# Kernel optimization log

Measured on AMD Instinct MI355X. Metric: run time of the kernel, lower is better.

Reference implementation:

```python
import jax, jax.numpy as jnp
import numpy as np

N, F, H, T = 100000, 128, 128, 10
E = 1600000
NUM_GRAPHS = 512
BN_EPS = 1e-5


def setup_inputs() -> dict:
    key = jax.random.key(0)
    ks = jax.random.split(key, 16)
    x = jax.random.normal(ks[0], (N, F), dtype=jnp.float32)
    edge_index = jax.random.randint(ks[1], (2, E), 0, N, dtype=jnp.int64)
    batch = jnp.sort(jax.random.randint(ks[2], (N,), 0, NUM_GRAPHS, dtype=jnp.int64))
    s = lambda fin: 1.0 / np.sqrt(fin)
    return {
        "x": x, "edge_index": edge_index, "batch": batch,
        # GINConv 1 MLP: Linear(F,H) -> BN(H) -> ReLU -> Linear(H,H)
        "W1a": jax.random.uniform(ks[3], (F, H), jnp.float32, -s(F), s(F)),
        "b1a": jax.random.uniform(ks[4], (H,), jnp.float32, -s(F), s(F)),
        "g1": jnp.ones((H,), jnp.float32),
        "bt1": jnp.zeros((H,), jnp.float32),
        "W1b": jax.random.uniform(ks[5], (H, H), jnp.float32, -s(H), s(H)),
        "b1b": jax.random.uniform(ks[6], (H,), jnp.float32, -s(H), s(H)),
        # GINConv 2 MLP
        "W2a": jax.random.uniform(ks[7], (H, H), jnp.float32, -s(H), s(H)),
        "b2a": jax.random.uniform(ks[8], (H,), jnp.float32, -s(H), s(H)),
        "g2": jnp.ones((H,), jnp.float32),
        "bt2": jnp.zeros((H,), jnp.float32),
        "W2b": jax.random.uniform(ks[9], (H, H), jnp.float32, -s(H), s(H)),
        "b2b": jax.random.uniform(ks[10], (H,), jnp.float32, -s(H), s(H)),
        # final Linear(H, T)
        "Wl": jax.random.uniform(ks[11], (H, T), jnp.float32, -s(H), s(H)),
        "bl": jax.random.uniform(ks[12], (T,), jnp.float32, -s(H), s(H)),
    }


def _batchnorm(h, gamma, beta):
    # training-mode BN over the node dimension (biased variance), eps=1e-5
    mean = jnp.mean(h, axis=0)
    var = jnp.mean(jnp.square(h - mean), axis=0)
    return (h - mean) * jax.lax.rsqrt(var + BN_EPS) * gamma + beta


def _gin_conv(x, edge_index, Wa, ba, gamma, beta, Wb, bb):
    src, dst = edge_index[0], edge_index[1]
    # sum-aggregate neighbor messages: scatter-add x[src] into dst rows
    agg = jax.ops.segment_sum(x[src], dst, num_segments=x.shape[0])
    h = (x + agg) @ Wa + ba          # eps=0 in GINConv default
    h = jax.nn.relu(_batchnorm(h, gamma, beta))
    return h @ Wb + bb


def reference(x, edge_index, batch, W1a, b1a, g1, bt1, W1b, b1b,
              W2a, b2a, g2, bt2, W2b, b2b, Wl, bl):
    h = jax.nn.relu(_gin_conv(x, edge_index, W1a, b1a, g1, bt1, W1b, b1b))
    h = jax.nn.relu(_gin_conv(h, edge_index, W2a, b2a, g2, bt2, W2b, b2b))
    pooled = jax.ops.segment_sum(h, batch, num_segments=NUM_GRAPHS)  # [G, H]
    return pooled @ Wl + bl  # [G, T]
```

## Files before the change

kernel.cpp:

```cpp
#include <hip/hip_runtime.h>
#include <cstdint>
#include <cstddef>

#define NFEAT 128
#define TGRAPH 10
#define NGRAPHS 512
#define BN_EPS 1e-5f
#define BIN_CHUNK 2048
#define GSPAN 8
#define TSTR 24

typedef __attribute__((ext_vector_type(8))) short bf16x8;
typedef __attribute__((ext_vector_type(4))) float f32x4;
typedef __attribute__((ext_vector_type(2))) float f32x2;

__device__ __forceinline__ float bf2f(short s) {
    union { unsigned u; float f; } c;
    c.u = ((unsigned)(unsigned short)s) << 16;
    return c.f;
}
__device__ __forceinline__ short f2bf(float f) {
    union { float f; unsigned u; } c;
    c.f = f;
    unsigned u = c.u;
    return (short)((u + 0x7fffu + ((u >> 16) & 1u)) >> 16);
}
__device__ __forceinline__ void accp(f32x2& a, unsigned v) {
    union { unsigned u; float f; } lo, hi;
    lo.u = v << 16;
    hi.u = v & 0xffff0000u;
    f32x2 t;
    t[0] = lo.f;
    t[1] = hi.f;
    a += t;
}


__global__ void k_bucket_scan(const int* __restrict__ bhist, int* __restrict__ bbase,
                              int* __restrict__ cur256, int E) {
    __shared__ int s[256];
    int t = threadIdx.x;
    int v = bhist[t];
    s[t] = v;
    __syncthreads();
    for (int off = 1; off < 256; off <<= 1) {
        int x = 0;
        if (t >= off) x = s[t - off];
        __syncthreads();
        if (t >= off) s[t] += x;
        __syncthreads();
    }
    int excl = s[t] - v;
    bbase[t] = excl;
    cur256[t] = excl;
    if (t == 255) bbase[256] = E;
}

__global__ __launch_bounds__(256) void k_bin_scatter(const int* __restrict__ src,
                                                     const int* __restrict__ dst,
                                                     int* __restrict__ cur256,
                                                     int2* __restrict__ binned, int E) {
    __shared__ int hist[256];
    __shared__ int base[256];
    int t = threadIdx.x;
    int e0 = blockIdx.x * BIN_CHUNK;
    int e1 = min(e0 + BIN_CHUNK, E);
    hist[t] = 0;
    __syncthreads();
    for (int e = e0 + t; e < e1; e += 256) {
        int b = dst[e] >> 9;
        atomicAdd(&hist[b], 1);
    }
    __syncthreads();
    int c = hist[t];
    if (c > 0) base[t] = atomicAdd(&cur256[t], c);
    __syncthreads();
    hist[t] = 0;
    __syncthreads();
    for (int e = e0 + t; e < e1; e += 256) {
        int d = dst[e];
        int b = d >> 9;
        int loc = atomicAdd(&hist[b], 1);
        binned[base[b] + loc] = make_int2(src[e], d);
    }
}

__global__ __launch_bounds__(512) void k_bucket_csr(const int2* __restrict__ binned,
                                                    const int* __restrict__ bbase,
                                                    int* __restrict__ rowptr,
                                                    int* __restrict__ adj,
                                                    int N, int E, int nb) {
    __shared__ int deg[512];
    __shared__ int cur[512];
    int b = blockIdx.x;
    int t = threadIdx.x;
    int e0 = bbase[b], e1 = bbase[b + 1];
    deg[t] = 0;
    __syncthreads();
    for (int e = e0 + t; e < e1; e += 512)
        atomicAdd(&deg[binned[e].y & 511], 1);
    __syncthreads();
    int v = deg[t];
    for (int off = 1; off < 512; off <<= 1) {
        int x = 0;
        if (t >= off) x = deg[t - off];
        __syncthreads();
        if (t >= off) deg[t] += x;
        __syncthreads();
    }
    int excl = deg[t] - v;
    cur[t] = excl;
    int node = b * 512 + t;
    if (node < N) rowptr[node] = e0 + excl;
    if (b == nb - 1 && t == 0) rowptr[N] = E;
    __syncthreads();
    for (int e = e0 + t; e < e1; e += 512) {
        int2 p = binned[e];
        int loc = atomicAdd(&cur[p.y & 511], 1);
        adj[e0 + loc] = p.x;
    }
}

__global__ __launch_bounds__(256) void k_prep_hist(const int* __restrict__ dst,
                                                   int* __restrict__ bhist, int E, int hb,
                                                   const float* __restrict__ x,
                                                   short* __restrict__ xbf,
                                                   const float* __restrict__ W0,
                                                   const float* __restrict__ W1,
                                                   const float* __restrict__ W2,
                                                   const float* __restrict__ W3,
                                                   short* __restrict__ Wf, int n4) {
    int t = threadIdx.x;
    if (blockIdx.x < hb) {
        __shared__ int h[256];
        h[t] = 0;
        __syncthreads();
        for (int e = blockIdx.x * 256 + t; e < E; e += hb * 256)
            atomicAdd(&h[dst[e] >> 9], 1);
        __syncthreads();
        if (h[t]) atomicAdd(&bhist[t], h[t]);
        return;
    }
    int i = (blockIdx.x - hb) * 256 + t;
    if (i < n4) {
        float4 v = ((const float4*)x)[i];
        ushort4 o;
        o.x = (unsigned short)f2bf(v.x);
        o.y = (unsigned short)f2bf(v.y);
        o.z = (unsigned short)f2bf(v.z);
        o.w = (unsigned short)f2bf(v.w);
        ((ushort4*)xbf)[i] = o;
    } else {
        int idx = i - n4;
        if (idx < 4 * 16384) {
            int w = idx >> 14, r = idx & 16383;
            int j = r & 7, lane = (r >> 3) & 63, ct = (r >> 9) & 7, kc = r >> 12;
            int k = kc * 32 + (lane >> 4) * 8 + j;
            int n = ct * 16 + (lane & 15);
            const float* W = (w == 0) ? W0 : (w == 1) ? W1 : (w == 2) ? W2 : W3;
            Wf[idx] = f2bf(W[k * NFEAT + n]);
        }
    }
}

__global__ __launch_bounds__(256) void k_aggregate_v4(const short* __restrict__ X,
                                                      const int* __restrict__ rowptr,
                                                      const int* __restrict__ adj,
                                                      short* __restrict__ XA, int N) {
    int tid = threadIdx.x;
    int lane = tid & 63;
    int g = lane >> 4;
    int p = lane & 15;
    int wid = (blockIdx.x * blockDim.x + tid) >> 6;
    if (wid >= N) return;
    const uint4* Xv = (const uint4*)X;
    f32x2 ac[4];
#pragma unroll
    for (int j = 0; j < 4; j++) ac[j] = (f32x2){0.f, 0.f};
    int r0 = rowptr[wid], r1 = rowptr[wid + 1];
    for (int e = r0; e < r1; e += 16) {
        int ea = e + g, eb = e + 4 + g, ec = e + 8 + g, ed = e + 12 + g;
        uint4 v0 = {0u, 0u, 0u, 0u}, v1 = {0u, 0u, 0u, 0u};
        uint4 v2 = {0u, 0u, 0u, 0u}, v3 = {0u, 0u, 0u, 0u};
        if (ea < r1) v0 = Xv[(size_t)adj[ea] * 16 + p];
        if (eb < r1) v1 = Xv[(size_t)adj[eb] * 16 + p];
        if (ec < r1) v2 = Xv[(size_t)adj[ec] * 16 + p];
        if (ed < r1) v3 = Xv[(size_t)adj[ed] * 16 + p];
        accp(ac[0], v0.x); accp(ac[1], v0.y); accp(ac[2], v0.z); accp(ac[3], v0.w);
        accp(ac[0], v1.x); accp(ac[1], v1.y); accp(ac[2], v1.z); accp(ac[3], v1.w);
        accp(ac[0], v2.x); accp(ac[1], v2.y); accp(ac[2], v2.z); accp(ac[3], v2.w);
        accp(ac[0], v3.x); accp(ac[1], v3.y); accp(ac[2], v3.z); accp(ac[3], v3.w);
    }
#pragma unroll
    for (int j = 0; j < 4; j++) {
        ac[j][0] += __shfl_xor(ac[j][0], 16);
        ac[j][1] += __shfl_xor(ac[j][1], 16);
        ac[j][0] += __shfl_xor(ac[j][0], 32);
        ac[j][1] += __shfl_xor(ac[j][1], 32);
    }
    if (g == 0) {
        uint4 sv = Xv[(size_t)wid * 16 + p];
        accp(ac[0], sv.x); accp(ac[1], sv.y); accp(ac[2], sv.z); accp(ac[3], sv.w);
        uint4 o;
        o.x = (unsigned)(unsigned short)f2bf(ac[0][0]) | ((unsigned)(unsigned short)f2bf(ac[0][1]) << 16);
        o.y = (unsigned)(unsigned short)f2bf(ac[1][0]) | ((unsigned)(unsigned short)f2bf(ac[1][1]) << 16);
        o.z = (unsigned)(unsigned short)f2bf(ac[2][0]) | ((unsigned)(unsigned short)f2bf(ac[2][1]) << 16);
        o.w = (unsigned)(unsigned short)f2bf(ac[3][0]) | ((unsigned)(unsigned short)f2bf(ac[3][1]) << 16);
        size_t dst = ((size_t)(wid >> 4) * 4 + (p >> 2)) * 512 +
                     (size_t)(((p & 3) * 16 + (wid & 15)) * 8);
        *(uint4*)(XA + dst) = o;
    }
}

template <bool BN_RELU_IN, bool RELU_OUT, bool STATS, bool FRAG_OUT, bool POOL>
__global__ __launch_bounds__(256) void k_gemm_mfma(const short* __restrict__ A,
                                                   const short* __restrict__ Wf,
                                                   const float* __restrict__ bias,
                                                   float* __restrict__ stats,
                                                   const float* __restrict__ gamma,
                                                   const float* __restrict__ beta,
                                                   const int* __restrict__ batch,
                                                   float* __restrict__ pooled,
                                                   short* __restrict__ C, int N) {
    __shared__ float s_aux[256];
    __shared__ short c_tile[4][32 * TSTR];
    __shared__ float s_pool[GSPAN][NFEAT];
    int tid = threadIdx.x;
    int wave = tid >> 6, lane = tid & 63;
    int quad = lane >> 4, l16 = lane & 15;
    int row_base = blockIdx.x * 128 + wave * 32;

    int gbase = 0;
    if constexpr (POOL) {
        int first = blockIdx.x * 128;
        gbase = (first < N) ? batch[first] : 0;
        for (int i = tid; i < GSPAN * NFEAT; i += 256) s_pool[i >> 7][i & 127] = 0.f;
    }
    if constexpr (STATS) s_aux[tid] = 0.f;
    if constexpr (BN_RELU_IN) {
        if (tid < NFEAT) {
            float mean = stats[tid] / (float)N;
            float var = stats[NFEAT + tid] / (float)N - mean * mean;
            float inv = rsqrtf(var + BN_EPS);
            float sc = gamma[tid] * inv;
            s_aux[tid] = sc;
            s_aux[NFEAT + tid] = beta[tid] - mean * sc;
        }
    }
    if constexpr (STATS || BN_RELU_IN || POOL) __syncthreads();

    f32x4 acc[2][8];
#pragma unroll
    for (int i = 0; i < 2; i++)
#pragma unroll
        for (int j = 0; j < 8; j++) acc[i][j] = (f32x4){0.f, 0.f, 0.f, 0.f};

    const short* af = A + ((size_t)(blockIdx.x * 8 + wave * 2) * 4) * 512;

#pragma unroll
    for (int kc = 0; kc < 4; ++kc) {
        bf16x8 a0 = *(const bf16x8*)(af + (size_t)kc * 512 + lane * 8);
        bf16x8 a1 = *(const bf16x8*)(af + (size_t)(4 + kc) * 512 + lane * 8);
        if constexpr (BN_RELU_IN) {
            int koff = kc * 32 + quad * 8;
#pragma unroll
            for (int j = 0; j < 8; j++) {
                float sc = s_aux[koff + j];
                float sh = s_aux[NFEAT + koff + j];
                a0[j] = f2bf(fmaxf(bf2f(a0[j]) * sc + sh, 0.f));
                a1[j] = f2bf(fmaxf(bf2f(a1[j]) * sc + sh, 0.f));
            }
        }
        const short* wp = Wf + ((size_t)(kc * 8) * 64 + lane) * 8;
#pragma unroll
        for (int ct = 0; ct < 8; ++ct) {
            bf16x8 b = *(const bf16x8*)(wp + (size_t)ct * 64 * 8);
            acc[0][ct] = __builtin_amdgcn_mfma_f32_16x16x32_bf16(a0, b, acc[0][ct], 0, 0, 0);
            acc[1][ct] = __builtin_amdgcn_mfma_f32_16x16x32_bf16(a1, b, acc[1][ct], 0, 0, 0);
        }
    }

    int dg[8];
    if constexpr (POOL) {
#pragma unroll
        for (int rt = 0; rt < 2; ++rt)
#pragma unroll
            for (int reg = 0; reg < 4; ++reg) {
                int row = row_base + rt * 16 + quad * 4 + reg;
                dg[rt * 4 + reg] = (row < N) ? (batch[row] - gbase) : -1;
            }
    }

    short* tile = &c_tile[wave][0];
    int row2 = lane >> 1, half = lane & 1;
#pragma unroll
    for (int ct = 0; ct < 8; ++ct) {
        int col = ct * 16 + l16;
        float bv = bias[col];
        float ls = 0.f, ls2 = 0.f;
        int cg = -1;
        float ps = 0.f;
#pragma unroll
        for (int rt = 0; rt < 2; ++rt) {
#pragma unroll
            for (int reg = 0; reg < 4; ++reg) {
                int lrow = rt * 16 + quad * 4 + reg;
                float v = acc[rt][ct][reg] + bv;
                if constexpr (RELU_OUT) v = fmaxf(v, 0.f);
                if constexpr (STATS) {
                    if (row_base + lrow < N) { ls += v; ls2 += v * v; }
                }
                if constexpr (POOL) {
                    int d = dg[rt * 4 + reg];
                    if (d != cg) {
                        if (cg >= 0) atomicAdd(&s_pool[cg & (GSPAN - 1)][col], ps);
                        cg = d; ps = 0.f;
                    }
                    if (d >= 0) ps += v;
                } else {
                    tile[lrow * TSTR + l16] = f2bf(v);
                }
            }
        }
        if constexpr (POOL) {
            if (cg >= 0) atomicAdd(&s_pool[cg & (GSPAN - 1)][col], ps);
        }
        if constexpr (STATS) {
            ls += __shfl_xor(ls, 16);
            ls += __shfl_xor(ls, 32);
            ls2 += __shfl_xor(ls2, 16);
            ls2 += __shfl_xor(ls2, 32);
            if (quad == 0) {
                atomicAdd(&s_aux[col], ls);
                atomicAdd(&s_aux[NFEAT + col], ls2);
            }
        }
        if constexpr (!POOL) {
            uint4 val = *(const uint4*)(tile + row2 * TSTR + half * 8);
            int grow = row_base + row2;
            if (grow < N) {
                int col0 = ct * 16 + half * 8;
                if constexpr (FRAG_OUT) {
                    size_t addr = ((size_t)(grow >> 4) * 4 + (col0 >> 5)) * 512 +
                                  (size_t)((((col0 >> 3) & 3) * 16 + (grow & 15)) * 8);
                    *(uint4*)(C + addr) = val;
                } else {
                    *(uint4*)(C + (size_t)grow * NFEAT + col0) = val;
                }
            }
        }
    }

    if constexpr (STATS) {
        __syncthreads();
        if (tid < NFEAT) {
            atomicAdd(&stats[tid], s_aux[tid]);
            atomicAdd(&stats[NFEAT + tid], s_aux[NFEAT + tid]);
        }
    }
    if constexpr (POOL) {
        __syncthreads();
        for (int i = tid; i < GSPAN * NFEAT; i += 256) {
            float v = s_pool[i >> 7][i & 127];
            if (v != 0.f) {
                int gg = gbase + (i >> 7);
                if (gg < NGRAPHS) atomicAdd(&pooled[gg * NFEAT + (i & 127)], v);
            }
        }
    }
}

__global__ void k_final(const float* __restrict__ pooled, const float* __restrict__ Wl,
                        const float* __restrict__ bl, float* __restrict__ out) {
    int idx = blockIdx.x * blockDim.x + threadIdx.x;
    if (idx >= NGRAPHS * TGRAPH) return;
    int g = idx / TGRAPH, t = idx % TGRAPH;
    const float* p = pooled + (size_t)g * NFEAT;
    float acc = bl[t];
#pragma unroll 16
    for (int k = 0; k < NFEAT; ++k) acc += p[k] * Wl[k * TGRAPH + t];
    out[idx] = acc;
}

extern "C" void kernel_launch(void* const* d_in, const int* in_sizes, int n_in,
                              void* d_out, int out_size, void* d_ws, size_t ws_size,
                              hipStream_t stream) {
    const float* x = (const float*)d_in[0];
    const int* ei = (const int*)d_in[1];
    const int* batch = (const int*)d_in[2];
    const float* W1a = (const float*)d_in[3];
    const float* b1a = (const float*)d_in[4];
    const float* g1 = (const float*)d_in[5];
    const float* bt1 = (const float*)d_in[6];
    const float* W1b = (const float*)d_in[7];
    const float* b1b = (const float*)d_in[8];
    const float* W2a = (const float*)d_in[9];
    const float* b2a = (const float*)d_in[10];
    const float* g2 = (const float*)d_in[11];
    const float* bt2 = (const float*)d_in[12];
    const float* W2b = (const float*)d_in[13];
    const float* b2b = (const float*)d_in[14];
    const float* Wl = (const float*)d_in[15];
    const float* bl = (const float*)d_in[16];
    float* out = (float*)d_out;

    int N = in_sizes[2];
    int E = in_sizes[1] / 2;
    int nb = (N + 511) >> 9;
    const int* src = ei;
    const int* dst = ei + E;

    int gemmBlocks = (N + 127) / 128;
    int padRows = gemmBlocks * 128;

    char* ws = (char*)d_ws;
    size_t off = 0;
    auto alloc = [&](size_t bytes) -> void* {
        void* p = ws + off;
        off = (off + bytes + 255) & ~(size_t)255;
        return p;
    };
    short* xbf = (short*)alloc((size_t)N * NFEAT * 2);
    short* ag = (short*)alloc((size_t)padRows * NFEAT * 2);
    short* ybf = (short*)alloc((size_t)padRows * NFEAT * 2);
    short* hbf = (short*)alloc((size_t)N * NFEAT * 2);
    short* Wf = (short*)alloc((size_t)4 * 16384 * 2);
    int* adj = (int*)alloc((size_t)E * 4);
    int2* binned = (int2*)alloc((size_t)E * 8);
    int* rowptr = (int*)alloc((size_t)(N + 1) * 4);
    int* bbase = (int*)alloc(257 * 4);
    int* cur256 = (int*)alloc(256 * 4);
    int* bhist = (int*)alloc(256 * 4);
    float* stats1 = (float*)alloc(256 * 4);
    float* stats2 = (float*)alloc(256 * 4);
    float* pooled = (float*)alloc((size_t)NGRAPHS * NFEAT * 4);
    size_t zbytes = (char*)(pooled + (size_t)NGRAPHS * NFEAT) - (char*)bhist;

    hipMemsetAsync(bhist, 0, zbytes, stream);

    int n4 = N * NFEAT / 4;
    int prepTot = n4 + 4 * 16384;
    int hb = 784;
    k_prep_hist<<<hb + (prepTot + 255) / 256, 256, 0, stream>>>(
        dst, bhist, E, hb, x, xbf, W1a, W1b, W2a, W2b, Wf, n4);
    k_bucket_scan<<<1, 256, 0, stream>>>(bhist, bbase, cur256, E);
    k_bin_scatter<<<(E + BIN_CHUNK - 1) / BIN_CHUNK, 256, 0, stream>>>(src, dst, cur256, binned, E);
    k_bucket_csr<<<nb, 512, 0, stream>>>(binned, bbase, rowptr, adj, N, E, nb);

    int aggBlocks = (N + 3) / 4;

    k_aggregate_v4<<<aggBlocks, 256, 0, stream>>>(xbf, rowptr, adj, ag, N);
    k_gemm_mfma<false, false, true, true, false><<<gemmBlocks, 256, 0, stream>>>(
        ag, Wf + 0 * 16384, b1a, stats1, nullptr, nullptr, nullptr, nullptr, ybf, N);
    k_gemm_mfma<true, true, false, false, false><<<gemmBlocks, 256, 0, stream>>>(
        ybf, Wf + 1 * 16384, b1b, stats1, g1, bt1, nullptr, nullptr, hbf, N);

    k_aggregate_v4<<<aggBlocks, 256, 0, stream>>>(hbf, rowptr, adj, ag, N);
    k_gemm_mfma<false, false, true, true, false><<<gemmBlocks, 256, 0, stream>>>(
        ag, Wf + 2 * 16384, b2a, stats2, nullptr, nullptr, nullptr, nullptr, ybf, N);
    k_gemm_mfma<true, true, false, false, true><<<gemmBlocks, 256, 0, stream>>>(
        ybf, Wf + 3 * 16384, b2b, stats2, g2, bt2, batch, pooled, nullptr, N);

    k_final<<<(NGRAPHS * TGRAPH + 255) / 256, 256, 0, stream>>>(pooled, Wl, bl, out);
}
```

Measured before the change: 440.9 us.

## Fuse neighbor aggregation into the first MLP GEMM of each GIN layer

Replaces the separate aggregation kernel and first GEMM with one kernel. Each lane gathers and sums neighbor rows straight into MFMA A-fragments in registers, then runs the bf16 MFMA and writes out bias, BN statistics and fragment-layout output. This removes the intermediate aggregated buffer round-trip through memory and one launch per layer. The trade-off is less memory-level parallelism in the gather: each lane walks a row's edges serially, and the grid is much smaller than the per-node-wave aggregation.

```diff
diff --git a/kernel.cpp b/kernel.cpp
--- a/kernel.cpp
+++ b/kernel.cpp
@@ -163,52 +163,137 @@
     }
 }
 
-__global__ __launch_bounds__(256) void k_aggregate_v4(const short* __restrict__ X,
-                                                      const int* __restrict__ rowptr,
-                                                      const int* __restrict__ adj,
-                                                      short* __restrict__ XA, int N) {
+__global__ __launch_bounds__(256) void k_agg_gemm(const short* __restrict__ X,
+                                                  const int* __restrict__ rowptr,
+                                                  const int* __restrict__ adj,
+                                                  const short* __restrict__ Wf,
+                                                  const float* __restrict__ bias,
+                                                  float* __restrict__ stats,
+                                                  short* __restrict__ C, int N) {
+    __shared__ float s_aux[256];
+    __shared__ short c_tile[4][32 * TSTR];
     int tid = threadIdx.x;
-    int lane = tid & 63;
-    int g = lane >> 4;
-    int p = lane & 15;
-    int wid = (blockIdx.x * blockDim.x + tid) >> 6;
-    if (wid >= N) return;
+    int wave = tid >> 6, lane = tid & 63;
+    int quad = lane >> 4, l16 = lane & 15;
+    int row_base = blockIdx.x * 128 + wave * 32;
+
+    s_aux[tid] = 0.f;
+    __syncthreads();
+
     const uint4* Xv = (const uint4*)X;
-    f32x2 ac[4];
-#pragma unroll
-    for (int j = 0; j < 4; j++) ac[j] = (f32x2){0.f, 0.f};
-    int r0 = rowptr[wid], r1 = rowptr[wid + 1];
-    for (int e = r0; e < r1; e += 16) {
-        int ea = e + g, eb = e + 4 + g, ec = e + 8 + g, ed = e + 12 + g;
-        uint4 v0 = {0u, 0u, 0u, 0u}, v1 = {0u, 0u, 0u, 0u};
-        uint4 v2 = {0u, 0u, 0u, 0u}, v3 = {0u, 0u, 0u, 0u};
-        if (ea < r1) v0 = Xv[(size_t)adj[ea] * 16 + p];
-        if (eb < r1) v1 = Xv[(size_t)adj[eb] * 16 + p];
-        if (ec < r1) v2 = Xv[(size_t)adj[ec] * 16 + p];
-        if (ed < r1) v3 = Xv[(size_t)adj[ed] * 16 + p];
-        accp(ac[0], v0.x); accp(ac[1], v0.y); accp(ac[2], v0.z); accp(ac[3], v0.w);
-        accp(ac[0], v1.x); accp(ac[1], v1.y); accp(ac[2], v1.z); accp(ac[3], v1.w);
-        accp(ac[0], v2.x); accp(ac[1], v2.y); accp(ac[2], v2.z); accp(ac[3], v2.w);
-        accp(ac[0], v3.x); accp(ac[1], v3.y); accp(ac[2], v3.z); accp(ac[3], v3.w);
-    }
-#pragma unroll
-    for (int j = 0; j < 4; j++) {
-        ac[j][0] += __shfl_xor(ac[j][0], 16);
-        ac[j][1] += __shfl_xor(ac[j][1], 16);
-        ac[j][0] += __shfl_xor(ac[j][0], 32);
-        ac[j][1] += __shfl_xor(ac[j][1], 32);
-    }
-    if (g == 0) {
-        uint4 sv = Xv[(size_t)wid * 16 + p];
-        accp(ac[0], sv.x); accp(ac[1], sv.y); accp(ac[2], sv.z); accp(ac[3], sv.w);
-        uint4 o;
-        o.x = (unsigned)(unsigned short)f2bf(ac[0][0]) | ((unsigned)(unsigned short)f2bf(ac[0][1]) << 16);
-        o.y = (unsigned)(unsigned short)f2bf(ac[1][0]) | ((unsigned)(unsigned short)f2bf(ac[1][1]) << 16);
-        o.z = (unsigned)(unsigned short)f2bf(ac[2][0]) | ((unsigned)(unsigned short)f2bf(ac[2][1]) << 16);
-        o.w = (unsigned)(unsigned short)f2bf(ac[3][0]) | ((unsigned)(unsigned short)f2bf(ac[3][1]) << 16);
-        size_t dst = ((size_t)(wid >> 4) * 4 + (p >> 2)) * 512 +
-                     (size_t)(((p & 3) * 16 + (wid & 15)) * 8);
-        *(uint4*)(XA + dst) = o;
+
+    bf16x8 afrag[2][4];
+#pragma unroll
+    for (int rt = 0; rt < 2; ++rt) {
+        f32x2 acc[4][4];
+#pragma unroll
+        for (int kc = 0; kc < 4; ++kc)
+#pragma unroll
+            for (int m = 0; m < 4; ++m) acc[kc][m] = (f32x2){0.f, 0.f};
+        int r = row_base + rt * 16 + l16;
+        if (r < N) {
+            size_t rb = (size_t)r * 16 + quad;
+#pragma unroll
+            for (int kc = 0; kc < 4; ++kc) {
+                uint4 v = Xv[rb + kc * 4];
+                accp(acc[kc][0], v.x); accp(acc[kc][1], v.y);
+                accp(acc[kc][2], v.z); accp(acc[kc][3], v.w);
+            }
+            int e = rowptr[r], e1 = rowptr[r + 1];
+            for (; e + 2 <= e1; e += 2) {
+                size_t n0 = (size_t)adj[e] * 16 + quad;
+                size_t n1 = (size_t)adj[e + 1] * 16 + quad;
+                uint4 u0[4], u1[4];
+#pragma unroll
+                for (int kc = 0; kc < 4; ++kc) u0[kc] = Xv[n0 + kc * 4];
+#pragma unroll
+                for (int kc = 0; kc < 4; ++kc) u1[kc] = Xv[n1 + kc * 4];
+#pragma unroll
+                for (int kc = 0; kc < 4; ++kc) {
+                    accp(acc[kc][0], u0[kc].x); accp(acc[kc][1], u0[kc].y);
+                    accp(acc[kc][2], u0[kc].z); accp(acc[kc][3], u0[kc].w);
+                    accp(acc[kc][0], u1[kc].x); accp(acc[kc][1], u1[kc].y);
+                    accp(acc[kc][2], u1[kc].z); accp(acc[kc][3], u1[kc].w);
+                }
+            }
+            if (e < e1) {
+                size_t n0 = (size_t)adj[e] * 16 + quad;
+#pragma unroll
+                for (int kc = 0; kc < 4; ++kc) {
+                    uint4 v = Xv[n0 + kc * 4];
+                    accp(acc[kc][0], v.x); accp(acc[kc][1], v.y);
+                    accp(acc[kc][2], v.z); accp(acc[kc][3], v.w);
+                }
+            }
+        }
+#pragma unroll
+        for (int kc = 0; kc < 4; ++kc) {
+            bf16x8 f;
+#pragma unroll
+            for (int m = 0; m < 4; ++m) {
+                f[2 * m] = f2bf(acc[kc][m][0]);
+                f[2 * m + 1] = f2bf(acc[kc][m][1]);
+            }
+            afrag[rt][kc] = f;
+        }
+    }
+
+    f32x4 acc[2][8];
+#pragma unroll
+    for (int i = 0; i < 2; i++)
+#pragma unroll
+        for (int j = 0; j < 8; j++) acc[i][j] = (f32x4){0.f, 0.f, 0.f, 0.f};
+
+#pragma unroll
+    for (int kc = 0; kc < 4; ++kc) {
+        const short* wp = Wf + ((size_t)(kc * 8) * 64 + lane) * 8;
+#pragma unroll
+        for (int ct = 0; ct < 8; ++ct) {
+            bf16x8 b = *(const bf16x8*)(wp + (size_t)ct * 64 * 8);
+            acc[0][ct] = __builtin_amdgcn_mfma_f32_16x16x32_bf16(afrag[0][kc], b, acc[0][ct], 0, 0, 0);
+            acc[1][ct] = __builtin_amdgcn_mfma_f32_16x16x32_bf16(afrag[1][kc], b, acc[1][ct], 0, 0, 0);
+        }
+    }
+
+    short* tile = &c_tile[wave][0];
+    int row2 = lane >> 1, half = lane & 1;
+#pragma unroll
+    for (int ct = 0; ct < 8; ++ct) {
+        int col = ct * 16 + l16;
+        float bv = bias[col];
+        float ls = 0.f, ls2 = 0.f;
+#pragma unroll
+        for (int rt = 0; rt < 2; ++rt) {
+#pragma unroll
+            for (int reg = 0; reg < 4; ++reg) {
+                int lrow = rt * 16 + quad * 4 + reg;
+                float v = acc[rt][ct][reg] + bv;
+                if (row_base + lrow < N) { ls += v; ls2 += v * v; }
+                tile[lrow * TSTR + l16] = f2bf(v);
+            }
+        }
+        ls += __shfl_xor(ls, 16);
+        ls += __shfl_xor(ls, 32);
+        ls2 += __shfl_xor(ls2, 16);
+        ls2 += __shfl_xor(ls2, 32);
+        if (quad == 0) {
+            atomicAdd(&s_aux[col], ls);
+            atomicAdd(&s_aux[NFEAT + col], ls2);
+        }
+        uint4 val = *(const uint4*)(tile + row2 * TSTR + half * 8);
+        int grow = row_base + row2;
+        if (grow < N) {
+            int col0 = ct * 16 + half * 8;
+            size_t addr = ((size_t)(grow >> 4) * 4 + (col0 >> 5)) * 512 +
+                          (size_t)((((col0 >> 3) & 3) * 16 + (grow & 15)) * 8);
+            *(uint4*)(C + addr) = val;
+        }
+    }
+
+    __syncthreads();
+    if (tid < NFEAT) {
+        atomicAdd(&stats[tid], s_aux[tid]);
+        atomicAdd(&stats[NFEAT + tid], s_aux[NFEAT + tid]);
     }
 }
 
@@ -421,7 +506,6 @@
         return p;
     };
     short* xbf = (short*)alloc((size_t)N * NFEAT * 2);
-    short* ag = (short*)alloc((size_t)padRows * NFEAT * 2);
     short* ybf = (short*)alloc((size_t)padRows * NFEAT * 2);
     short* hbf = (short*)alloc((size_t)N * NFEAT * 2);
     short* Wf = (short*)alloc((size_t)4 * 16384 * 2);
@@ -447,17 +531,13 @@
     k_bin_scatter<<<(E + BIN_CHUNK - 1) / BIN_CHUNK, 256, 0, stream>>>(src, dst, cur256, binned, E);
     k_bucket_csr<<<nb, 512, 0, stream>>>(binned, bbase, rowptr, adj, N, E, nb);
 
-    int aggBlocks = (N + 3) / 4;
-
-    k_aggregate_v4<<<aggBlocks, 256, 0, stream>>>(xbf, rowptr, adj, ag, N);
-    k_gemm_mfma<false, false, true, true, false><<<gemmBlocks, 256, 0, stream>>>(
-        ag, Wf + 0 * 16384, b1a, stats1, nullptr, nullptr, nullptr, nullptr, ybf, N);
+    k_agg_gemm<<<gemmBlocks, 256, 0, stream>>>(xbf, rowptr, adj, Wf + 0 * 16384, b1a,
+                                               stats1, ybf, N);
     k_gemm_mfma<true, true, false, false, false><<<gemmBlocks, 256, 0, stream>>>(
         ybf, Wf + 1 * 16384, b1b, stats1, g1, bt1, nullptr, nullptr, hbf, N);
 
-    k_aggregate_v4<<<aggBlocks, 256, 0, stream>>>(hbf, rowptr, adj, ag, N);
-    k_gemm_mfma<false, false, true, true, false><<<gemmBlocks, 256, 0, stream>>>(
-        ag, Wf + 2 * 16384, b2a, stats2, nullptr, nullptr, nullptr, nullptr, ybf, N);
+    k_agg_gemm<<<gemmBlocks, 256, 0, stream>>>(hbf, rowptr, adj, Wf + 2 * 16384, b2a,
+                                               stats2, ybf, N);
     k_gemm_mfma<true, true, false, false, true><<<gemmBlocks, 256, 0, stream>>>(
         ybf, Wf + 3 * 16384, b2b, stats2, g2, bt2, batch, pooled, nullptr, N);
 
```

New measurement: 452.4 us. 1.03x slower.

## Fuse neighbor aggregation with first MLP GEMM and BN stats

Applied to the files above, without the earlier changes.

Replaces the separate aggregation kernel and first GEMM with one kernel. Each 1024-thread block aggregates 16 rows into shared memory, then 8 waves run MFMA for the 16x128 output tile, add bias, accumulate batch-norm statistics and write fragment-layout output. This removes the round trip of the aggregated intermediate through global memory and one launch per layer. In exchange it adds a block-wide sync per 16 rows and many more stats atomics, since blocks now cover 16 rows instead of 128.

```diff
diff --git a/kernel.cpp b/kernel.cpp
--- a/kernel.cpp
+++ b/kernel.cpp
@@ -163,33 +163,40 @@
     }
 }
 
-__global__ __launch_bounds__(256) void k_aggregate_v4(const short* __restrict__ X,
-                                                      const int* __restrict__ rowptr,
-                                                      const int* __restrict__ adj,
-                                                      short* __restrict__ XA, int N) {
+__global__ __launch_bounds__(1024, 8) void k_agg_gemm_a(const short* __restrict__ X,
+                                                        const int* __restrict__ rowptr,
+                                                        const int* __restrict__ adj,
+                                                        const short* __restrict__ Wf,
+                                                        const float* __restrict__ bias,
+                                                        float* __restrict__ stats,
+                                                        short* __restrict__ C, int N) {
+    __shared__ __align__(16) short arow[16][136];
+    __shared__ __align__(16) short c_tile[8][16 * TSTR];
+    __shared__ float s_aux[256];
     int tid = threadIdx.x;
-    int lane = tid & 63;
-    int g = lane >> 4;
-    int p = lane & 15;
-    int wid = (blockIdx.x * blockDim.x + tid) >> 6;
-    if (wid >= N) return;
+    int wave = tid >> 6, lane = tid & 63;
+    int g = lane >> 4, p = lane & 15;
+    int wid = blockIdx.x * 16 + wave;
+
     const uint4* Xv = (const uint4*)X;
     f32x2 ac[4];
 #pragma unroll
     for (int j = 0; j < 4; j++) ac[j] = (f32x2){0.f, 0.f};
-    int r0 = rowptr[wid], r1 = rowptr[wid + 1];
-    for (int e = r0; e < r1; e += 16) {
-        int ea = e + g, eb = e + 4 + g, ec = e + 8 + g, ed = e + 12 + g;
-        uint4 v0 = {0u, 0u, 0u, 0u}, v1 = {0u, 0u, 0u, 0u};
-        uint4 v2 = {0u, 0u, 0u, 0u}, v3 = {0u, 0u, 0u, 0u};
-        if (ea < r1) v0 = Xv[(size_t)adj[ea] * 16 + p];
-        if (eb < r1) v1 = Xv[(size_t)adj[eb] * 16 + p];
-        if (ec < r1) v2 = Xv[(size_t)adj[ec] * 16 + p];
-        if (ed < r1) v3 = Xv[(size_t)adj[ed] * 16 + p];
-        accp(ac[0], v0.x); accp(ac[1], v0.y); accp(ac[2], v0.z); accp(ac[3], v0.w);
-        accp(ac[0], v1.x); accp(ac[1], v1.y); accp(ac[2], v1.z); accp(ac[3], v1.w);
-        accp(ac[0], v2.x); accp(ac[1], v2.y); accp(ac[2], v2.z); accp(ac[3], v2.w);
-        accp(ac[0], v3.x); accp(ac[1], v3.y); accp(ac[2], v3.z); accp(ac[3], v3.w);
+    if (wid < N) {
+        int r0 = rowptr[wid], r1 = rowptr[wid + 1];
+        for (int e = r0; e < r1; e += 16) {
+            int ea = e + g, eb = e + 4 + g, ec = e + 8 + g, ed = e + 12 + g;
+            uint4 v0 = {0u, 0u, 0u, 0u}, v1 = {0u, 0u, 0u, 0u};
+            uint4 v2 = {0u, 0u, 0u, 0u}, v3 = {0u, 0u, 0u, 0u};
+            if (ea < r1) v0 = Xv[(size_t)adj[ea] * 16 + p];
+            if (eb < r1) v1 = Xv[(size_t)adj[eb] * 16 + p];
+            if (ec < r1) v2 = Xv[(size_t)adj[ec] * 16 + p];
+            if (ed < r1) v3 = Xv[(size_t)adj[ed] * 16 + p];
+            accp(ac[0], v0.x); accp(ac[1], v0.y); accp(ac[2], v0.z); accp(ac[3], v0.w);
+            accp(ac[0], v1.x); accp(ac[1], v1.y); accp(ac[2], v1.z); accp(ac[3], v1.w);
+            accp(ac[0], v2.x); accp(ac[1], v2.y); accp(ac[2], v2.z); accp(ac[3], v2.w);
+            accp(ac[0], v3.x); accp(ac[1], v3.y); accp(ac[2], v3.z); accp(ac[3], v3.w);
+        }
     }
 #pragma unroll
     for (int j = 0; j < 4; j++) {
@@ -199,16 +206,60 @@
         ac[j][1] += __shfl_xor(ac[j][1], 32);
     }
     if (g == 0) {
-        uint4 sv = Xv[(size_t)wid * 16 + p];
-        accp(ac[0], sv.x); accp(ac[1], sv.y); accp(ac[2], sv.z); accp(ac[3], sv.w);
+        if (wid < N) {
+            uint4 sv = Xv[(size_t)wid * 16 + p];
+            accp(ac[0], sv.x); accp(ac[1], sv.y); accp(ac[2], sv.z); accp(ac[3], sv.w);
+        }
         uint4 o;
         o.x = (unsigned)(unsigned short)f2bf(ac[0][0]) | ((unsigned)(unsigned short)f2bf(ac[0][1]) << 16);
         o.y = (unsigned)(unsigned short)f2bf(ac[1][0]) | ((unsigned)(unsigned short)f2bf(ac[1][1]) << 16);
         o.z = (unsigned)(unsigned short)f2bf(ac[2][0]) | ((unsigned)(unsigned short)f2bf(ac[2][1]) << 16);
         o.w = (unsigned)(unsigned short)f2bf(ac[3][0]) | ((unsigned)(unsigned short)f2bf(ac[3][1]) << 16);
-        size_t dst = ((size_t)(wid >> 4) * 4 + (p >> 2)) * 512 +
-                     (size_t)(((p & 3) * 16 + (wid & 15)) * 8);
-        *(uint4*)(XA + dst) = o;
+        *(uint4*)&arow[wave][p * 8] = o;
+    }
+    __syncthreads();
+
+    if (wave < 8) {
+        int ct = wave;
+        f32x4 oacc = (f32x4){0.f, 0.f, 0.f, 0.f};
+#pragma unroll
+        for (int kc = 0; kc < 4; ++kc) {
+            bf16x8 a = *(const bf16x8*)&arow[p][kc * 32 + g * 8];
+            bf16x8 b = *(const bf16x8*)(Wf + (size_t)kc * 4096 + (size_t)ct * 512 + lane * 8);
+            oacc = __builtin_amdgcn_mfma_f32_16x16x32_bf16(a, b, oacc, 0, 0, 0);
+        }
+        int col = ct * 16 + p;
+        float bv = bias[col];
+        float ls = 0.f, ls2 = 0.f;
+        short* tl = &c_tile[wave][0];
+#pragma unroll
+        for (int reg = 0; reg < 4; ++reg) {
+            int lrow = g * 4 + reg;
+            float v = oacc[reg] + bv;
+            if (blockIdx.x * 16 + lrow < N) { ls += v; ls2 += v * v; }
+            tl[lrow * TSTR + p] = f2bf(v);
+        }
+        ls += __shfl_xor(ls, 16);
+        ls += __shfl_xor(ls, 32);
+        ls2 += __shfl_xor(ls2, 16);
+        ls2 += __shfl_xor(ls2, 32);
+        if (g == 0) {
+            s_aux[col] = ls;
+            s_aux[NFEAT + col] = ls2;
+        }
+        if (lane < 32) {
+            int row2 = lane >> 1, half = lane & 1;
+            uint4 val = *(const uint4*)(tl + row2 * TSTR + half * 8);
+            int col0 = ct * 16 + half * 8;
+            size_t addr = ((size_t)blockIdx.x * 4 + (col0 >> 5)) * 512 +
+                          (size_t)((((col0 >> 3) & 3) * 16 + row2) * 8);
+            *(uint4*)(C + addr) = val;
+        }
+    }
+    __syncthreads();
+    if (tid < NFEAT) {
+        atomicAdd(&stats[tid], s_aux[tid]);
+        atomicAdd(&stats[NFEAT + tid], s_aux[NFEAT + tid]);
     }
 }
 
@@ -223,7 +274,7 @@
                                                    float* __restrict__ pooled,
                                                    short* __restrict__ C, int N) {
     __shared__ float s_aux[256];
-    __shared__ short c_tile[4][32 * TSTR];
+    __shared__ __align__(16) short c_tile[4][32 * TSTR];
     __shared__ float s_pool[GSPAN][NFEAT];
     int tid = threadIdx.x;
     int wave = tid >> 6, lane = tid & 63;
@@ -412,6 +463,7 @@
 
     int gemmBlocks = (N + 127) / 128;
     int padRows = gemmBlocks * 128;
+    int aggBlocks16 = (N + 15) / 16;
 
     char* ws = (char*)d_ws;
     size_t off = 0;
@@ -421,7 +473,6 @@
         return p;
     };
     short* xbf = (short*)alloc((size_t)N * NFEAT * 2);
-    short* ag = (short*)alloc((size_t)padRows * NFEAT * 2);
     short* ybf = (short*)alloc((size_t)padRows * NFEAT * 2);
     short* hbf = (short*)alloc((size_t)N * NFEAT * 2);
     short* Wf = (short*)alloc((size_t)4 * 16384 * 2);
@@ -447,17 +498,13 @@
     k_bin_scatter<<<(E + BIN_CHUNK - 1) / BIN_CHUNK, 256, 0, stream>>>(src, dst, cur256, binned, E);
     k_bucket_csr<<<nb, 512, 0, stream>>>(binned, bbase, rowptr, adj, N, E, nb);
 
-    int aggBlocks = (N + 3) / 4;
-
-    k_aggregate_v4<<<aggBlocks, 256, 0, stream>>>(xbf, rowptr, adj, ag, N);
-    k_gemm_mfma<false, false, true, true, false><<<gemmBlocks, 256, 0, stream>>>(
-        ag, Wf + 0 * 16384, b1a, stats1, nullptr, nullptr, nullptr, nullptr, ybf, N);
+    k_agg_gemm_a<<<aggBlocks16, 1024, 0, stream>>>(xbf, rowptr, adj, Wf + 0 * 16384, b1a,
+                                                   stats1, ybf, N);
     k_gemm_mfma<true, true, false, false, false><<<gemmBlocks, 256, 0, stream>>>(
         ybf, Wf + 1 * 16384, b1b, stats1, g1, bt1, nullptr, nullptr, hbf, N);
 
-    k_aggregate_v4<<<aggBlocks, 256, 0, stream>>>(hbf, rowptr, adj, ag, N);
-    k_gemm_mfma<false, false, true, true, false><<<gemmBlocks, 256, 0, stream>>>(
-        ag, Wf + 2 * 16384, b2a, stats2, nullptr, nullptr, nullptr, nullptr, ybf, N);
+    k_agg_gemm_a<<<aggBlocks16, 1024, 0, stream>>>(hbf, rowptr, adj, Wf + 2 * 16384, b2a,
+                                                   stats2, ybf, N);
     k_gemm_mfma<true, true, false, false, true><<<gemmBlocks, 256, 0, stream>>>(
         ybf, Wf + 3 * 16384, b2b, stats2, g2, bt2, batch, pooled, nullptr, N);
 
```

Measured after the change: 577.8 us. +31.0%, slower.
